# Kernel optimization log

Hardware: AMD Instinct MI355X
Metric: run time of the kernel (lower is better)

The kernel has to match this reference:

```python
import jax, jax.numpy as jnp
import numpy as np

N = 50000
E = 800000
F_IN = 64
HID = 64
NCLS = 16


def setup_inputs() -> dict:
    key = jax.random.key(0)
    ks = jax.random.split(key, 8)
    x = jax.random.normal(ks[0], (N, F_IN), dtype=jnp.float32)
    edge_index = jax.random.randint(ks[1], (2, E), 0, N, dtype=jnp.int64)
    edge_weight = jax.random.uniform(ks[2], (E,), dtype=jnp.float32)
    # GCNConv glorot-style weights (PyG stores weight as [in, out]) and zero bias
    W1 = jax.random.normal(ks[3], (F_IN, HID), dtype=jnp.float32) * (1.0 / np.sqrt(F_IN))
    b1 = jnp.zeros((HID,), dtype=jnp.float32)
    W2 = jax.random.normal(ks[4], (HID, HID), dtype=jnp.float32) * (1.0 / np.sqrt(HID))
    b2 = jnp.zeros((HID,), dtype=jnp.float32)
    Wout = jax.random.normal(ks[5], (HID, NCLS), dtype=jnp.float32) * (1.0 / np.sqrt(HID))
    bout = jnp.zeros((NCLS,), dtype=jnp.float32)
    return {"x": x, "edge_index": edge_index, "edge_weight": edge_weight,
            "W1": W1, "b1": b1, "W2": W2, "b2": b2, "Wout": Wout, "bout": bout}


def _gcn_norm(edge_index, edge_weight, num_nodes):
    # PyG gcn_norm with add_self_loops=True (self-loop weight = 1.0)
    row = jnp.concatenate([edge_index[0], jnp.arange(num_nodes, dtype=edge_index.dtype)])
    col = jnp.concatenate([edge_index[1], jnp.arange(num_nodes, dtype=edge_index.dtype)])
    w = jnp.concatenate([edge_weight, jnp.ones((num_nodes,), dtype=edge_weight.dtype)])
    deg = jax.ops.segment_sum(w, col, num_segments=num_nodes)  # [N]
    dinv = jnp.where(deg > 0, jax.lax.rsqrt(deg), 0.0)
    norm = dinv[row] * w * dinv[col]  # [E+N]
    return row, col, norm


def _gcn_conv(h, row, col, norm, W, b, num_nodes):
    h = h @ W                                   # [N, out]
    msg = h[row] * norm[:, None]                # gather + scale, [E+N, out]
    out = jax.ops.segment_sum(msg, col, num_segments=num_nodes)  # scatter-add
    return out + b


def reference(x, edge_index, edge_weight, W1, b1, W2, b2, Wout, bout):
    num_nodes = x.shape[0]
    row, col, norm = _gcn_norm(edge_index, edge_weight, num_nodes)
    h = _gcn_conv(x, row, col, norm, W1, b1, num_nodes)
    h = jax.nn.relu(h)  # dropout is identity in eval mode
    h = _gcn_conv(h, row, col, norm, W2, b2, num_nodes)
    h = jax.nn.relu(h)
    logits = h @ Wout + bout
    return jax.nn.softmax(logits, axis=1)
```

## Files before the change

kernel.cpp:

```cpp
#include <hip/hip_runtime.h>
#include <math.h>

#define NN 50000
#define NE 800000
#define F 64
#define NCLS 16

#define BKS 7
#define BKN 128
#define NBK 391
#define B1C 4096
#define B1B 196
#define CAP2 3072

typedef unsigned short u16;
typedef __attribute__((ext_vector_type(8))) unsigned short ushort8v;

__device__ __forceinline__ float bf2f(u16 h) {
    return __uint_as_float((unsigned)h << 16);
}
__device__ __forceinline__ u16 f2bf(float f) {
    unsigned u = __float_as_uint(f);
    return (u16)((u + 0x7fffu + ((u >> 16) & 1u)) >> 16);
}

__global__ void k_zeroi(int* __restrict__ p, int n) {
    int i = blockIdx.x * 256 + threadIdx.x;
    if (i < n) p[i] = 0;
}


__global__ __launch_bounds__(256) void k_bkhist(const int* __restrict__ col,
                                                int* __restrict__ bkcnt) {
    __shared__ int h[NBK];
    for (int i = threadIdx.x; i < NBK; i += 256) h[i] = 0;
    __syncthreads();
    int stride = gridDim.x * 256;
    for (int e = blockIdx.x * 256 + threadIdx.x; e < NE; e += stride)
        atomicAdd(&h[col[e] >> BKS], 1);
    __syncthreads();
    for (int i = threadIdx.x; i < NBK; i += 256) {
        int v = h[i];
        if (v) atomicAdd(&bkcnt[i], v);
    }
}


__global__ __launch_bounds__(512) void k_scan_bk(const int* __restrict__ bkcnt,
                                                 int* __restrict__ bkbase,
                                                 int* __restrict__ bkcur) {
    __shared__ int sa[512], sb[512];
    int t = threadIdx.x;
    int c = (t < NBK) ? bkcnt[t] : 0;
    sa[t] = c;
    __syncthreads();
    int* src = sa; int* dst = sb;
#pragma unroll
    for (int off = 1; off < 512; off <<= 1) {
        dst[t] = src[t] + ((t >= off) ? src[t - off] : 0);
        __syncthreads();
        int* tq = src; src = dst; dst = tq;
    }
    if (t < NBK) {
        int excl = src[t] - c;
        bkbase[t] = excl;
        bkcur[t]  = excl;
    }
    if (t == NBK) bkbase[t] = NE;
}


__global__ __launch_bounds__(512) void k_bucket1(const int* __restrict__ row,
                                                 const int* __restrict__ col,
                                                 const float* __restrict__ w,
                                                 int* __restrict__ bkcur,
                                                 int2* __restrict__ tmp) {
    __shared__ int hist[512];
    __shared__ int sa[512], sb[512];
    __shared__ int lbase[512];
    __shared__ int gbase[512];
    __shared__ int lcur[512];
    __shared__ int2 stage[B1C];
    int t = threadIdx.x;
    int e0 = blockIdx.x * B1C;
    int cnt = min(B1C, NE - e0);
    hist[t] = 0;
    __syncthreads();

    int mykey[8]; int myb[8]; int myw[8]; bool myv[8];
#pragma unroll
    for (int k = 0; k < 8; ++k) {
        int i = t + k * 512;
        myv[k] = (i < cnt);
        if (myv[k]) {
            int e = e0 + i;
            int c = col[e];
            myb[k]   = c >> BKS;
            mykey[k] = (row[e] << BKS) | (c & (BKN - 1));
            myw[k]   = __float_as_int(w[e]);
            atomicAdd(&hist[myb[k]], 1);
        }
    }
    __syncthreads();

    sa[t] = hist[t];
    __syncthreads();
    int* src = sa; int* dst = sb;
#pragma unroll
    for (int off = 1; off < 512; off <<= 1) {
        dst[t] = src[t] + ((t >= off) ? src[t - off] : 0);
        __syncthreads();
        int* tq = src; src = dst; dst = tq;
    }
    int lex = src[t] - hist[t];
    lbase[t] = lex;
    lcur[t]  = lex;
    gbase[t] = (t < NBK && hist[t] > 0) ? atomicAdd(&bkcur[t], hist[t]) : 0;
    __syncthreads();

#pragma unroll
    for (int k = 0; k < 8; ++k) {
        if (myv[k]) {
            int pos = atomicAdd(&lcur[myb[k]], 1);
            stage[pos] = make_int2(mykey[k], myw[k]);
        }
    }
    __syncthreads();

    for (int i = t; i < cnt; i += 512) {
        int lo = 0, hi = NBK;
        while (hi - lo > 1) {
            int mid = (lo + hi) >> 1;
            if (lbase[mid] <= i) lo = mid; else hi = mid;
        }
        tmp[gbase[lo] + (i - lbase[lo])] = stage[i];
    }
}


__global__ __launch_bounds__(256) void k_bucket2(const int* __restrict__ bkbase,
                                                 const int2* __restrict__ tmp,
                                                 int2* __restrict__ sedge,
                                                 int* __restrict__ incl,
                                                 float* __restrict__ dinv) {
    __shared__ int2 stage[CAP2];
    __shared__ int2 sorted[CAP2];
    __shared__ int hist[BKN];
    __shared__ int sa[BKN], sb[BKN];
    __shared__ int lcur[BKN];
    int b = blockIdx.x;
    int t = threadIdx.x;
    int rbeg = bkbase[b], rend = bkbase[b + 1];
    int cnt = min(rend - rbeg, CAP2);
    if (t < BKN) hist[t] = 0;
    __syncthreads();
    for (int i = t; i < cnt; i += 256) {
        int2 ed = tmp[rbeg + i];
        stage[i] = ed;
        atomicAdd(&hist[ed.x & (BKN - 1)], 1);
    }
    __syncthreads();
    if (t < BKN) sa[t] = hist[t];
    __syncthreads();
    int* src = sa; int* dst = sb;
#pragma unroll
    for (int off = 1; off < BKN; off <<= 1) {
        if (t < BKN) dst[t] = src[t] + ((t >= off) ? src[t - off] : 0);
        __syncthreads();
        int* tq = src; src = dst; dst = tq;
    }
    int node0 = b * BKN;
    int lincl = 0, lexcl = 0;
    if (t < BKN) {
        lincl = src[t];
        lexcl = lincl - hist[t];
        lcur[t] = lexcl;
        if (node0 + t < NN) incl[node0 + t] = rbeg + lincl;
    }
    __syncthreads();
    for (int i = t; i < cnt; i += 256) {
        int2 ed = stage[i];
        int pos = atomicAdd(&lcur[ed.x & (BKN - 1)], 1);
        sorted[pos] = ed;
    }
    __syncthreads();
    if (t < BKN && node0 + t < NN) {
        float s = 1.0f;
        for (int e = lexcl; e < lincl; ++e) s += __int_as_float(sorted[e].y);
        dinv[node0 + t] = rsqrtf(s);
    }
    for (int i = t; i < cnt; i += 256) {
        int2 ed = sorted[i];
        sedge[rbeg + i] = make_int2(ed.x >> BKS, ed.y);
    }
}


template<bool BF>
__global__ __launch_bounds__(256) void k_mm64(const void* __restrict__ Xv,
                                              const float* __restrict__ W,
                                              u16* __restrict__ Y) {
    __shared__ float sW[64 * 64];
    __shared__ float sX[16][64];
    int tid = threadIdx.x;
    int c  = tid & 63;
    int wv = tid >> 6;
    for (int i = tid; i < 64 * 64; i += 256) sW[i] = W[i];
    int r0 = blockIdx.x * 16;
#pragma unroll
    for (int i = tid; i < 16 * 64; i += 256) {
        size_t idx = (size_t)(r0 + (i >> 6)) * 64 + (i & 63);
        if (BF) sX[i >> 6][i & 63] = bf2f(((const u16*)Xv)[idx]);
        else    sX[i >> 6][i & 63] = ((const float*)Xv)[idx];
    }
    __syncthreads();
    int rb = wv * 4;
    float a0 = 0.f, a1 = 0.f, a2 = 0.f, a3 = 0.f;
#pragma unroll
    for (int k = 0; k < 64; k += 4) {
        float4 x0 = *(const float4*)&sX[rb + 0][k];
        float4 x1 = *(const float4*)&sX[rb + 1][k];
        float4 x2 = *(const float4*)&sX[rb + 2][k];
        float4 x3 = *(const float4*)&sX[rb + 3][k];
        float wA = sW[(k + 0) * 64 + c];
        float wB = sW[(k + 1) * 64 + c];
        float wC = sW[(k + 2) * 64 + c];
        float wD = sW[(k + 3) * 64 + c];
        a0 += x0.x * wA + x0.y * wB + x0.z * wC + x0.w * wD;
        a1 += x1.x * wA + x1.y * wB + x1.z * wC + x1.w * wD;
        a2 += x2.x * wA + x2.y * wB + x2.z * wC + x2.w * wD;
        a3 += x3.x * wA + x3.y * wB + x3.z * wC + x3.w * wD;
    }
    Y[(size_t)(r0 + rb + 0) * 64 + c] = f2bf(a0);
    Y[(size_t)(r0 + rb + 1) * 64 + c] = f2bf(a1);
    Y[(size_t)(r0 + rb + 2) * 64 + c] = f2bf(a2);
    Y[(size_t)(r0 + rb + 3) * 64 + c] = f2bf(a3);
}


template<bool HEAD>
__global__ __launch_bounds__(256) void k_agg(const u16* __restrict__ A,
                                             const int* __restrict__ incl,
                                             const int2* __restrict__ sedge,
                                             const float* __restrict__ dinv,
                                             const float* __restrict__ bias,
                                             u16* __restrict__ B,
                                             const float* __restrict__ Wout,
                                             const float* __restrict__ bout,
                                             float* __restrict__ out) {
    __shared__ float sWout[64 * NCLS];
    __shared__ float sh[4][64];
    int tid  = threadIdx.x;
    int wv   = tid >> 6;
    int node = blockIdx.x * 4 + wv;
    int lane = tid & 63;
    int slot = lane >> 3;
    int fg   = lane & 7;
    if (HEAD) {
        for (int i = tid; i < 64 * NCLS; i += 256) sWout[i] = Wout[i];
    }
    int beg = (node == 0) ? 0 : incl[node - 1];
    int end = incl[node];
    int deg = end - beg;
    float acc[8] = {0.f, 0.f, 0.f, 0.f, 0.f, 0.f, 0.f, 0.f};
    for (int base = 0; base < deg; base += 64) {
        int i = base + lane;
        int2 ed = (i < deg) ? sedge[beg + i] : make_int2(0, 0);
        float nmr = __int_as_float(ed.y) * dinv[ed.x];
        int m = min(64, deg - base);
        int steps = (m + 7) >> 3;
        for (int t = 0; t < steps; ++t) {
            int idx = (t << 3) + slot;
            int   s  = __shfl(ed.x, idx);
            float nm = __shfl(nmr, idx);
            const ushort8v a = *(const ushort8v*)(A + (size_t)s * 64 + (fg << 3));
#pragma unroll
            for (int j = 0; j < 8; ++j) acc[j] += bf2f(a[j]) * nm;
        }
    }
#pragma unroll
    for (int o = 8; o <= 32; o <<= 1) {
#pragma unroll
        for (int j = 0; j < 8; ++j) acc[j] += __shfl_xor(acc[j], o);
    }
    float dc = dinv[node];
    if (slot == 0) {
        float d2 = dc * dc;
        const ushort8v self = *(const ushort8v*)(A + (size_t)node * 64 + (fg << 3));
        const float4 bb0 = *(const float4*)(bias + (fg << 3));
        const float4 bb1 = *(const float4*)(bias + (fg << 3) + 4);
        float bbv[8] = {bb0.x, bb0.y, bb0.z, bb0.w, bb1.x, bb1.y, bb1.z, bb1.w};
        ushort8v ov;
#pragma unroll
        for (int j = 0; j < 8; ++j) {
            float v = fmaxf(acc[j] * dc + bf2f(self[j]) * d2 + bbv[j], 0.f);
            ov[j] = f2bf(v);
            if (HEAD) sh[wv][(fg << 3) + j] = v;
        }
        *(ushort8v*)(B + (size_t)node * 64 + (fg << 3)) = ov;
    }
    if (HEAD) {
        __syncthreads();
        int c = lane & 15, q = lane >> 4;
        float p = 0.f;
#pragma unroll
        for (int k = 0; k < 16; ++k)
            p += sh[wv][q * 16 + k] * sWout[(q * 16 + k) * NCLS + c];
        p += __shfl_xor(p, 16);
        p += __shfl_xor(p, 32);
        p += bout[c];
        float mx = p;
#pragma unroll
        for (int o = 8; o >= 1; o >>= 1) mx = fmaxf(mx, __shfl_xor(mx, o, 16));
        float ex = expf(p - mx);
        float s = ex;
#pragma unroll
        for (int o = 8; o >= 1; o >>= 1) s += __shfl_xor(s, o, 16);
        if (lane < 16) out[(size_t)node * NCLS + c] = ex / s;
    }
}


extern "C" void kernel_launch(void* const* d_in, const int* in_sizes, int n_in,
                              void* d_out, int out_size, void* d_ws, size_t ws_size,
                              hipStream_t stream) {
    const float* x    = (const float*)d_in[0];
    const int*   ei   = (const int*)d_in[1];
    const float* ew   = (const float*)d_in[2];
    const float* W1   = (const float*)d_in[3];
    const float* b1   = (const float*)d_in[4];
    const float* W2   = (const float*)d_in[5];
    const float* b2   = (const float*)d_in[6];
    const float* Wout = (const float*)d_in[7];
    const float* bout = (const float*)d_in[8];
    const int* row = ei;
    const int* col = ei + NE;

    int*   ip     = (int*)d_ws;
    int*   incl   = ip;
    float* dinv   = (float*)(ip + 50048);
    int*   bkcnt  = ip + 100096;
    int*   bkbase = ip + 100608;
    int*   bkcur  = ip + 101120;
    int2*  sedge  = (int2*)(ip + 101632);
    u16*   A      = (u16*)(ip + 101632 + 2 * NE);
    u16*   B      = (u16*)(ip + 101632 + 2 * NE + 1600000);
    int2*  tmp    = (int2*)A;

    k_zeroi<<<2, 256, 0, stream>>>(bkcnt, 512);
    k_bkhist<<<B1B, 256, 0, stream>>>(col, bkcnt);
    k_scan_bk<<<1, 512, 0, stream>>>(bkcnt, bkbase, bkcur);
    k_bucket1<<<B1B, 512, 0, stream>>>(row, col, ew, bkcur, tmp);
    k_bucket2<<<NBK, 256, 0, stream>>>(bkbase, tmp, sedge, incl, dinv);

    k_mm64<false><<<NN / 16, 256, 0, stream>>>(x, W1, A);
    k_agg<false><<<NN / 4, 256, 0, stream>>>(A, incl, sedge, dinv, b1, B,
                                             nullptr, nullptr, nullptr);
    k_mm64<true><<<NN / 16, 256, 0, stream>>>(B, W2, A);
    k_agg<true><<<NN / 4, 256, 0, stream>>>(A, incl, sedge, dinv, b2, B,
                                            Wout, bout, (float*)d_out);
}
```

Baseline: 219.6 us.

## Replace bucket histogram+scan with fixed-capacity buckets; aggregate two nodes per wavefront

```diff
diff --git a/kernel.cpp b/kernel.cpp
--- a/kernel.cpp
+++ b/kernel.cpp
@@ -9,6 +9,7 @@
 #define BKS 7
 #define BKN 128
 #define NBK 391
+#define CAP 2560
 #define B1C 4096
 #define B1B 196
 #define CAP2 3072
@@ -24,49 +25,9 @@
     return (u16)((u + 0x7fffu + ((u >> 16) & 1u)) >> 16);
 }
 
-__global__ void k_zeroi(int* __restrict__ p, int n) {
-    int i = blockIdx.x * 256 + threadIdx.x;
-    if (i < n) p[i] = 0;
-}
-
-
-__global__ __launch_bounds__(256) void k_bkhist(const int* __restrict__ col,
-                                                int* __restrict__ bkcnt) {
-    __shared__ int h[NBK];
-    for (int i = threadIdx.x; i < NBK; i += 256) h[i] = 0;
-    __syncthreads();
-    int stride = gridDim.x * 256;
-    for (int e = blockIdx.x * 256 + threadIdx.x; e < NE; e += stride)
-        atomicAdd(&h[col[e] >> BKS], 1);
-    __syncthreads();
-    for (int i = threadIdx.x; i < NBK; i += 256) {
-        int v = h[i];
-        if (v) atomicAdd(&bkcnt[i], v);
-    }
-}
-
-
-__global__ __launch_bounds__(512) void k_scan_bk(const int* __restrict__ bkcnt,
-                                                 int* __restrict__ bkbase,
-                                                 int* __restrict__ bkcur) {
-    __shared__ int sa[512], sb[512];
-    int t = threadIdx.x;
-    int c = (t < NBK) ? bkcnt[t] : 0;
-    sa[t] = c;
-    __syncthreads();
-    int* src = sa; int* dst = sb;
-#pragma unroll
-    for (int off = 1; off < 512; off <<= 1) {
-        dst[t] = src[t] + ((t >= off) ? src[t - off] : 0);
-        __syncthreads();
-        int* tq = src; src = dst; dst = tq;
-    }
-    if (t < NBK) {
-        int excl = src[t] - c;
-        bkbase[t] = excl;
-        bkcur[t]  = excl;
-    }
-    if (t == NBK) bkbase[t] = NE;
+__global__ void k_init_cur(int* __restrict__ cur) {
+    int b = blockIdx.x * 256 + threadIdx.x;
+    if (b < NBK) cur[b] = b * CAP;
 }
 
 
@@ -138,10 +99,11 @@
 }
 
 
-__global__ __launch_bounds__(256) void k_bucket2(const int* __restrict__ bkbase,
+__global__ __launch_bounds__(256) void k_bucket2(const int* __restrict__ bkcur,
                                                  const int2* __restrict__ tmp,
                                                  int2* __restrict__ sedge,
-                                                 int* __restrict__ incl,
+                                                 int* __restrict__ begA,
+                                                 int* __restrict__ endA,
                                                  float* __restrict__ dinv) {
     __shared__ int2 stage[CAP2];
     __shared__ int2 sorted[CAP2];
@@ -150,8 +112,8 @@
     __shared__ int lcur[BKN];
     int b = blockIdx.x;
     int t = threadIdx.x;
-    int rbeg = bkbase[b], rend = bkbase[b + 1];
-    int cnt = min(rend - rbeg, CAP2);
+    int rbeg = b * CAP;
+    int cnt = min(bkcur[b] - rbeg, CAP2);
     if (t < BKN) hist[t] = 0;
     __syncthreads();
     for (int i = t; i < cnt; i += 256) {
@@ -175,7 +137,10 @@
         lincl = src[t];
         lexcl = lincl - hist[t];
         lcur[t] = lexcl;
-        if (node0 + t < NN) incl[node0 + t] = rbeg + lincl;
+        if (node0 + t < NN) {
+            begA[node0 + t] = rbeg + lexcl;
+            endA[node0 + t] = rbeg + lincl;
+        }
     }
     __syncthreads();
     for (int i = t; i < cnt; i += 256) {
@@ -240,7 +205,8 @@
 
 template<bool HEAD>
 __global__ __launch_bounds__(256) void k_agg(const u16* __restrict__ A,
-                                             const int* __restrict__ incl,
+                                             const int* __restrict__ begA,
+                                             const int* __restrict__ endA,
                                              const int2* __restrict__ sedge,
                                              const float* __restrict__ dinv,
                                              const float* __restrict__ bias,
@@ -249,28 +215,29 @@
                                              const float* __restrict__ bout,
                                              float* __restrict__ out) {
     __shared__ float sWout[64 * NCLS];
-    __shared__ float sh[4][64];
+    __shared__ float sh[8][64];
     int tid  = threadIdx.x;
     int wv   = tid >> 6;
-    int node = blockIdx.x * 4 + wv;
     int lane = tid & 63;
-    int slot = lane >> 3;
-    int fg   = lane & 7;
+    int half = lane >> 5;
+    int sub  = lane & 31;
+    int slot = sub >> 3;
+    int fg   = sub & 7;
+    int node = blockIdx.x * 8 + wv * 2 + half;
     if (HEAD) {
         for (int i = tid; i < 64 * NCLS; i += 256) sWout[i] = Wout[i];
     }
-    int beg = (node == 0) ? 0 : incl[node - 1];
-    int end = incl[node];
-    int deg = end - beg;
+    int beg = begA[node];
+    int deg = endA[node] - beg;
     float acc[8] = {0.f, 0.f, 0.f, 0.f, 0.f, 0.f, 0.f, 0.f};
-    for (int base = 0; base < deg; base += 64) {
-        int i = base + lane;
+    for (int base = 0; base < deg; base += 32) {
+        int i = base + sub;
         int2 ed = (i < deg) ? sedge[beg + i] : make_int2(0, 0);
         float nmr = __int_as_float(ed.y) * dinv[ed.x];
-        int m = min(64, deg - base);
-        int steps = (m + 7) >> 3;
+        int m = min(32, deg - base);
+        int steps = (m + 3) >> 2;
         for (int t = 0; t < steps; ++t) {
-            int idx = (t << 3) + slot;
+            int idx = (half << 5) + (t << 2) + slot;
             int   s  = __shfl(ed.x, idx);
             float nm = __shfl(nmr, idx);
             const ushort8v a = *(const ushort8v*)(A + (size_t)s * 64 + (fg << 3));
@@ -279,13 +246,13 @@
         }
     }
 #pragma unroll
-    for (int o = 8; o <= 32; o <<= 1) {
+    for (int o = 8; o <= 16; o <<= 1) {
 #pragma unroll
         for (int j = 0; j < 8; ++j) acc[j] += __shfl_xor(acc[j], o);
     }
-    float dc = dinv[node];
     if (slot == 0) {
-        float d2 = dc * dc;
+        float d = dinv[node];
+        float d2 = d * d;
         const ushort8v self = *(const ushort8v*)(A + (size_t)node * 64 + (fg << 3));
         const float4 bb0 = *(const float4*)(bias + (fg << 3));
         const float4 bb1 = *(const float4*)(bias + (fg << 3) + 4);
@@ -293,21 +260,23 @@
         ushort8v ov;
 #pragma unroll
         for (int j = 0; j < 8; ++j) {
-            float v = fmaxf(acc[j] * dc + bf2f(self[j]) * d2 + bbv[j], 0.f);
+            float v = fmaxf(acc[j] * d + bf2f(self[j]) * d2 + bbv[j], 0.f);
             ov[j] = f2bf(v);
-            if (HEAD) sh[wv][(fg << 3) + j] = v;
+            if (HEAD) sh[wv * 2 + half][(fg << 3) + j] = v;
         }
         *(ushort8v*)(B + (size_t)node * 64 + (fg << 3)) = ov;
     }
     if (HEAD) {
         __syncthreads();
-        int c = lane & 15, q = lane >> 4;
+        int nib  = tid >> 5;
+        int sub2 = tid & 31;
+        int c = sub2 & 15, q = sub2 >> 4;
+        const float* hrow = sh[nib];
         float p = 0.f;
 #pragma unroll
-        for (int k = 0; k < 16; ++k)
-            p += sh[wv][q * 16 + k] * sWout[(q * 16 + k) * NCLS + c];
+        for (int k = 0; k < 32; ++k)
+            p += hrow[q * 32 + k] * sWout[(q * 32 + k) * NCLS + c];
         p += __shfl_xor(p, 16);
-        p += __shfl_xor(p, 32);
         p += bout[c];
         float mx = p;
 #pragma unroll
@@ -316,7 +285,7 @@
         float s = ex;
 #pragma unroll
         for (int o = 8; o >= 1; o >>= 1) s += __shfl_xor(s, o, 16);
-        if (lane < 16) out[(size_t)node * NCLS + c] = ex / s;
+        if (q == 0) out[(size_t)(blockIdx.x * 8 + nib) * NCLS + c] = ex / s;
     }
 }
 
@@ -337,26 +306,23 @@
     const int* col = ei + NE;
 
     int*   ip     = (int*)d_ws;
-    int*   incl   = ip;
-    float* dinv   = (float*)(ip + 50048);
-    int*   bkcnt  = ip + 100096;
-    int*   bkbase = ip + 100608;
-    int*   bkcur  = ip + 101120;
-    int2*  sedge  = (int2*)(ip + 101632);
-    u16*   A      = (u16*)(ip + 101632 + 2 * NE);
-    u16*   B      = (u16*)(ip + 101632 + 2 * NE + 1600000);
+    int*   begA   = ip;
+    int*   endA   = ip + 50048;
+    float* dinv   = (float*)(ip + 100096);
+    int*   bkcur  = ip + 150144;
+    int2*  sedge  = (int2*)(ip + 150656);
+    u16*   A      = (u16*)(ip + 150656 + 2 * NBK * CAP);
+    u16*   B      = A + 3200000;
     int2*  tmp    = (int2*)A;
 
-    k_zeroi<<<2, 256, 0, stream>>>(bkcnt, 512);
-    k_bkhist<<<B1B, 256, 0, stream>>>(col, bkcnt);
-    k_scan_bk<<<1, 512, 0, stream>>>(bkcnt, bkbase, bkcur);
+    k_init_cur<<<2, 256, 0, stream>>>(bkcur);
     k_bucket1<<<B1B, 512, 0, stream>>>(row, col, ew, bkcur, tmp);
-    k_bucket2<<<NBK, 256, 0, stream>>>(bkbase, tmp, sedge, incl, dinv);
+    k_bucket2<<<NBK, 256, 0, stream>>>(bkcur, tmp, sedge, begA, endA, dinv);
 
     k_mm64<false><<<NN / 16, 256, 0, stream>>>(x, W1, A);
-    k_agg<false><<<NN / 4, 256, 0, stream>>>(A, incl, sedge, dinv, b1, B,
+    k_agg<false><<<NN / 8, 256, 0, stream>>>(A, begA, endA, sedge, dinv, b1, B,
                                              nullptr, nullptr, nullptr);
     k_mm64<true><<<NN / 16, 256, 0, stream>>>(B, W2, A);
-    k_agg<true><<<NN / 4, 256, 0, stream>>>(A, incl, sedge, dinv, b2, B,
+    k_agg<true><<<NN / 8, 256, 0, stream>>>(A, begA, endA, sedge, dinv, b2, B,
                                             Wout, bout, (float*)d_out);
 }
```

After: 188.2 us. 1.17x faster.
